# Kernel optimization log

Measured on AMD Instinct MI355X. Metric: run time of the kernel, lower is better.

Reference implementation:

```python
import jax, jax.numpy as jnp
import numpy as np

N = 8192
D_IN = 512
D_HID = 256
D_OUT = 128
NEG_SLOPE = 0.25
MASK_VAL = -1.0e12
EDGE_PROB = 0.004  # avg degree ~33


def _leaky(x):
    return jax.nn.leaky_relu(x, NEG_SLOPE)


def setup_inputs() -> dict:
    key = jax.random.key(0)
    ks = jax.random.split(key, 9)
    x = jax.random.normal(ks[0], (N, D_IN), jnp.float32)
    # sparse-ish normalized adjacency, stored dense (torch uses sparse mm / to_dense)
    vals = jax.random.uniform(ks[1], (N, N), jnp.float32)
    mask = jax.random.uniform(ks[2], (N, N)) < EDGE_PROB
    adj = jnp.where(mask, vals, 0.0).astype(jnp.float32)
    W1 = jax.random.normal(ks[3], (D_IN, D_HID), jnp.float32) * (2.0 / (D_IN + D_HID)) ** 0.5
    b1 = jnp.zeros((D_HID,), jnp.float32)
    W2 = jax.random.normal(ks[4], (D_HID, D_HID), jnp.float32) * (1.0 / D_HID) ** 0.5
    b2 = jnp.zeros((D_HID,), jnp.float32)
    Wg = jax.random.normal(ks[5], (D_HID, D_OUT), jnp.float32) * (2.0 / (D_HID + D_OUT)) ** 0.5
    a = jax.random.normal(ks[6], (2 * D_OUT, 1), jnp.float32) * 0.1
    return dict(x=x, adj=adj, W1=W1, b1=b1, W2=W2, b2=b2, Wg=Wg, a=a)


def reference(x, adj, W1, b1, W2, b2, Wg, a):
    # GCN layer 1: adj @ (x @ W1) + b1, leaky_relu (dropout p=0 / eval -> identity)
    x1 = _leaky(adj @ (x @ W1) + b1)
    # GCN layer 2
    x2 = _leaky(adj @ (x1 @ W2) + b2)
    # GAT layer: h = x2 @ Wg; e[i,j] = leaky_relu([h_i || h_j] @ a)
    # identical to leaky_relu((h@a1)_i + (h@a2)_j) without the O(N^2*2F) concat
    h = x2 @ Wg                              # [N, D_OUT]
    a1 = a[:D_OUT, 0]
    a2 = a[D_OUT:, 0]
    e = _leaky((h @ a1)[:, None] + (h @ a2)[None, :])  # [N, N]
    att = jnp.where(adj > 0, e, MASK_VAL)
    att = jax.nn.softmax(att, axis=1)
    h_prime = att @ h                        # [N, D_OUT] (concat=False -> no elu)
    out = _leaky(h_prime)
    mu = out[:, : D_OUT // 2]
    logvar = out[:, D_OUT // 2 :]
    return mu, logvar
```

## Files before the change

### kernel.cpp

```cpp
#include <hip/hip_runtime.h>

typedef unsigned short u16;
typedef u16 u16x4 __attribute__((ext_vector_type(4)));
typedef __bf16 bf16x8 __attribute__((ext_vector_type(8)));
typedef float f32x4 __attribute__((ext_vector_type(4)));

#define NROW 8192
#define CAP 128
#define D_IN 512
#define D_HID 256
#define D_OUT 128

__device__ __forceinline__ float leaky_f(float x) { return x > 0.f ? x : 0.25f * x; }

__device__ __forceinline__ u16 f2bf_rne(float f) {
  unsigned u = __float_as_uint(f);
  u += 0x7fffu + ((u >> 16) & 1u);
  return (u16)(u >> 16);
}
__device__ __forceinline__ float bf2f(u16 v) { return __uint_as_float(((unsigned)v) << 16); }
__device__ __forceinline__ void split_bf16(float f, u16& hi, u16& lo) {
  hi = f2bf_rne(f);
  float fh = __uint_as_float(((unsigned)hi) << 16);
  lo = f2bf_rne(f - fh);
}

__global__ __launch_bounds__(256) void k_packw(
    const float* __restrict__ W1, u16* __restrict__ B1,
    const float* __restrict__ W2, u16* __restrict__ B2,
    const float* __restrict__ Wg, u16* __restrict__ B3) {
  const float* W; u16* Bt; int K, Nc, idx;
  int pb = blockIdx.x;
  if (pb < 64)      { W = W1; Bt = B1; K = D_IN;  Nc = D_HID; idx = pb * 256 + threadIdx.x; }
  else if (pb < 96) { W = W2; Bt = B2; K = D_HID; Nc = D_HID; idx = (pb - 64) * 256 + threadIdx.x; }
  else              { W = Wg; Bt = B3; K = D_HID; Nc = D_OUT; idx = (pb - 96) * 256 + threadIdx.x; }
  int ko8 = K >> 3;
  int n = idx / ko8, k0 = (idx % ko8) << 3;
  alignas(16) u16 hh[8], ll[8];
#pragma unroll
  for (int j = 0; j < 8; ++j) {
    float f = W[(size_t)(k0 + j) * Nc + n];
    split_bf16(f, hh[j], ll[j]);
  }
  size_t ro = (size_t)n * 2 * K;
  *(uint4*)(Bt + ro + k0)     = *(const uint4*)hh;
  *(uint4*)(Bt + ro + K + k0) = *(const uint4*)ll;
}

__global__ __launch_bounds__(256) void k_csr_gemm1(const float* __restrict__ adj,
    int* __restrict__ cnt, int* __restrict__ cols, float* __restrict__ vals,
    const float* __restrict__ X, const u16* __restrict__ Bt, u16* __restrict__ C) {
  __shared__ alignas(16) u16 Ah[64 * 40], Al[64 * 40];
  __shared__ alignas(16) u16 Bh[64 * 40], Bl[64 * 40];
  __shared__ int csrc;
  int b = blockIdx.x;
  int tid = threadIdx.x;
  if (b < 512) {
    const int N = D_HID, K = D_IN;
    int bm = (b >> 2) * 64, bn = (b & 3) * 64;
    int wave = tid >> 6, lane = tid & 63, l15 = lane & 15, quad = lane >> 4;
    f32x4 acc[4] = {};
    int ar = tid >> 2, aj = (tid & 3) << 3;
    const float* Xrow = X + (size_t)(bm + ar) * K + aj;
    const u16* Brow = Bt + (size_t)(bn + ar) * (2 * K) + aj;
    for (int k0 = 0; k0 < K; k0 += 32) {
      alignas(16) u16 hh[8], ll[8];
      float xv[8];
      *(float4*)(xv)     = *(const float4*)(Xrow + k0);
      *(float4*)(xv + 4) = *(const float4*)(Xrow + k0 + 4);
#pragma unroll
      for (int e = 0; e < 8; ++e) split_bf16(xv[e], hh[e], ll[e]);
      *(uint4*)(&Ah[ar * 40 + aj]) = *(const uint4*)hh;
      *(uint4*)(&Al[ar * 40 + aj]) = *(const uint4*)ll;
      *(uint4*)(&Bh[ar * 40 + aj]) = *(const uint4*)(Brow + k0);
      *(uint4*)(&Bl[ar * 40 + aj]) = *(const uint4*)(Brow + K + k0);
      __syncthreads();
      bf16x8 afh = *(const bf16x8*)(&Ah[(wave * 16 + l15) * 40 + quad * 8]);
      bf16x8 afl = *(const bf16x8*)(&Al[(wave * 16 + l15) * 40 + quad * 8]);
#pragma unroll
      for (int c = 0; c < 4; ++c) {
        bf16x8 bfh = *(const bf16x8*)(&Bh[(c * 16 + l15) * 40 + quad * 8]);
        bf16x8 bfl = *(const bf16x8*)(&Bl[(c * 16 + l15) * 40 + quad * 8]);
        acc[c] = __builtin_amdgcn_mfma_f32_16x16x32_bf16(afh, bfh, acc[c], 0, 0, 0);
        acc[c] = __builtin_amdgcn_mfma_f32_16x16x32_bf16(afh, bfl, acc[c], 0, 0, 0);
        acc[c] = __builtin_amdgcn_mfma_f32_16x16x32_bf16(afl, bfh, acc[c], 0, 0, 0);
      }
      __syncthreads();
    }
#pragma unroll
    for (int c = 0; c < 4; ++c)
#pragma unroll
      for (int rg = 0; rg < 4; ++rg) {
        int rowi = bm + wave * 16 + quad * 4 + rg;
        int coli = bn + c * 16 + l15;
        C[(size_t)rowi * N + coli] = f2bf_rne(acc[c][rg]);
      }
    return;
  }
  int i = b - 512;
  if (tid == 0) csrc = 0;
  __syncthreads();
  int lane = tid & 63;
  const float4* row = (const float4*)(adj + (size_t)i * NROW);
  for (int j4 = tid; j4 < NROW / 4; j4 += 256) {
    float4 v = row[j4];
    int base = j4 * 4;
    bool p0 = v.x > 0.f, p1 = v.y > 0.f, p2 = v.z > 0.f, p3 = v.w > 0.f;
    unsigned long long m0 = __ballot(p0), m1 = __ballot(p1);
    unsigned long long m2 = __ballot(p2), m3 = __ballot(p3);
    int c0 = __popcll(m0), c1 = __popcll(m1), c2 = __popcll(m2), c3 = __popcll(m3);
    int tot = c0 + c1 + c2 + c3;
    if (tot) {
      int wbase = 0;
      if (lane == 0) wbase = atomicAdd(&csrc, tot);
      wbase = __shfl(wbase, 0);
      unsigned long long lm = (1ULL << lane) - 1ULL;
      int o0 = wbase + __popcll(m0 & lm);
      int o1 = wbase + c0 + __popcll(m1 & lm);
      int o2 = wbase + c0 + c1 + __popcll(m2 & lm);
      int o3 = wbase + c0 + c1 + c2 + __popcll(m3 & lm);
      if (p0 && o0 < CAP) { cols[i*CAP+o0] = base;   vals[i*CAP+o0] = v.x; }
      if (p1 && o1 < CAP) { cols[i*CAP+o1] = base+1; vals[i*CAP+o1] = v.y; }
      if (p2 && o2 < CAP) { cols[i*CAP+o2] = base+2; vals[i*CAP+o2] = v.z; }
      if (p3 && o3 < CAP) { cols[i*CAP+o3] = base+3; vals[i*CAP+o3] = v.w; }
    }
  }
  __syncthreads();
  if (tid == 0) cnt[i] = (csrc < CAP) ? csrc : CAP;
}


__device__ __forceinline__ float4 gather_row256(const u16* __restrict__ Hin,
    const int* scw, const float* svw, int n, int lane) {
  float4 acc = {0.f, 0.f, 0.f, 0.f};
  int k = 0;
  for (; k + 7 < n; k += 8) {
    int   c0 = scw[k],     c1 = scw[k + 1], c2 = scw[k + 2], c3 = scw[k + 3];
    int   c4 = scw[k + 4], c5 = scw[k + 5], c6 = scw[k + 6], c7 = scw[k + 7];
    float w0 = svw[k],     w1 = svw[k + 1], w2 = svw[k + 2], w3 = svw[k + 3];
    float w4 = svw[k + 4], w5 = svw[k + 5], w6 = svw[k + 6], w7 = svw[k + 7];
    u16x4 v0 = *(const u16x4*)(Hin + (size_t)c0 * 256 + 4 * lane);
    u16x4 v1 = *(const u16x4*)(Hin + (size_t)c1 * 256 + 4 * lane);
    u16x4 v2 = *(const u16x4*)(Hin + (size_t)c2 * 256 + 4 * lane);
    u16x4 v3 = *(const u16x4*)(Hin + (size_t)c3 * 256 + 4 * lane);
    u16x4 v4 = *(const u16x4*)(Hin + (size_t)c4 * 256 + 4 * lane);
    u16x4 v5 = *(const u16x4*)(Hin + (size_t)c5 * 256 + 4 * lane);
    u16x4 v6 = *(const u16x4*)(Hin + (size_t)c6 * 256 + 4 * lane);
    u16x4 v7 = *(const u16x4*)(Hin + (size_t)c7 * 256 + 4 * lane);
    acc.x = fmaf(w0, bf2f(v0[0]), acc.x); acc.y = fmaf(w0, bf2f(v0[1]), acc.y);
    acc.z = fmaf(w0, bf2f(v0[2]), acc.z); acc.w = fmaf(w0, bf2f(v0[3]), acc.w);
    acc.x = fmaf(w1, bf2f(v1[0]), acc.x); acc.y = fmaf(w1, bf2f(v1[1]), acc.y);
    acc.z = fmaf(w1, bf2f(v1[2]), acc.z); acc.w = fmaf(w1, bf2f(v1[3]), acc.w);
    acc.x = fmaf(w2, bf2f(v2[0]), acc.x); acc.y = fmaf(w2, bf2f(v2[1]), acc.y);
    acc.z = fmaf(w2, bf2f(v2[2]), acc.z); acc.w = fmaf(w2, bf2f(v2[3]), acc.w);
    acc.x = fmaf(w3, bf2f(v3[0]), acc.x); acc.y = fmaf(w3, bf2f(v3[1]), acc.y);
    acc.z = fmaf(w3, bf2f(v3[2]), acc.z); acc.w = fmaf(w3, bf2f(v3[3]), acc.w);
    acc.x = fmaf(w4, bf2f(v4[0]), acc.x); acc.y = fmaf(w4, bf2f(v4[1]), acc.y);
    acc.z = fmaf(w4, bf2f(v4[2]), acc.z); acc.w = fmaf(w4, bf2f(v4[3]), acc.w);
    acc.x = fmaf(w5, bf2f(v5[0]), acc.x); acc.y = fmaf(w5, bf2f(v5[1]), acc.y);
    acc.z = fmaf(w5, bf2f(v5[2]), acc.z); acc.w = fmaf(w5, bf2f(v5[3]), acc.w);
    acc.x = fmaf(w6, bf2f(v6[0]), acc.x); acc.y = fmaf(w6, bf2f(v6[1]), acc.y);
    acc.z = fmaf(w6, bf2f(v6[2]), acc.z); acc.w = fmaf(w6, bf2f(v6[3]), acc.w);
    acc.x = fmaf(w7, bf2f(v7[0]), acc.x); acc.y = fmaf(w7, bf2f(v7[1]), acc.y);
    acc.z = fmaf(w7, bf2f(v7[2]), acc.z); acc.w = fmaf(w7, bf2f(v7[3]), acc.w);
  }
  for (; k < n; ++k) {
    float wv = svw[k];
    u16x4 v = *(const u16x4*)(Hin + (size_t)scw[k] * 256 + 4 * lane);
    acc.x = fmaf(wv, bf2f(v[0]), acc.x); acc.y = fmaf(wv, bf2f(v[1]), acc.y);
    acc.z = fmaf(wv, bf2f(v[2]), acc.z); acc.w = fmaf(wv, bf2f(v[3]), acc.w);
  }
  return acc;
}

__global__ __launch_bounds__(256) void k_fuse1(const u16* __restrict__ Hin,
    const float* __restrict__ bias, const int* __restrict__ cnt,
    const int* __restrict__ cols, const float* __restrict__ vals,
    const u16* __restrict__ Bt, u16* __restrict__ Cout) {
  __shared__ alignas(16) u16 AhF[8 * 16 * 40], AlF[8 * 16 * 40];
  __shared__ int   sc[4 * CAP];
  __shared__ float sv[4 * CAP];
  int tid = threadIdx.x;
  int wave = tid >> 6, lane = tid & 63, l15 = lane & 15, quad = lane >> 4;
  int bm = blockIdx.x * 16;
  int* scw = sc + wave * CAP;
  float* svw = sv + wave * CAP;
  float4 bv = ((const float4*)bias)[lane];
#pragma unroll
  for (int rr = 0; rr < 4; ++rr) {
    int r = wave * 4 + rr;
    int i = bm + r;
    int n = cnt[i];
    if (lane < n)      { scw[lane]      = cols[i*CAP+lane];      svw[lane]      = vals[i*CAP+lane]; }
    if (lane + 64 < n) { scw[lane + 64] = cols[i*CAP+lane+64];   svw[lane + 64] = vals[i*CAP+lane+64]; }
    float4 acc = gather_row256(Hin, scw, svw, n, lane);
    float r4[4] = { leaky_f(acc.x + bv.x), leaky_f(acc.y + bv.y),
                    leaky_f(acc.z + bv.z), leaky_f(acc.w + bv.w) };
    u16x4 hi4, lo4;
#pragma unroll
    for (int e = 0; e < 4; ++e) { u16 hh, ll; split_bf16(r4[e], hh, ll); hi4[e] = hh; lo4[e] = ll; }
    int dst = (lane >> 3) * 640 + r * 40 + (lane & 7) * 4;
    *(u16x4*)(&AhF[dst]) = hi4;
    *(u16x4*)(&AlF[dst]) = lo4;
  }
  __syncthreads();
#pragma unroll
  for (int hN = 0; hN < 2; ++hN) {
    f32x4 acc[2] = {};
#pragma unroll
    for (int k0 = 0; k0 < D_HID; k0 += 32) {
      bf16x8 afh = *(const bf16x8*)(&AhF[(k0 >> 5) * 640 + l15 * 40 + quad * 8]);
      bf16x8 afl = *(const bf16x8*)(&AlF[(k0 >> 5) * 640 + l15 * 40 + quad * 8]);
#pragma unroll
      for (int c = 0; c < 2; ++c) {
        int col = hN * 128 + wave * 32 + c * 16 + l15;
        const u16* bp = Bt + (size_t)col * (2 * D_HID) + k0 + quad * 8;
        bf16x8 bfh = *(const bf16x8*)(bp);
        bf16x8 bfl = *(const bf16x8*)(bp + D_HID);
        acc[c] = __builtin_amdgcn_mfma_f32_16x16x32_bf16(afh, bfh, acc[c], 0, 0, 0);
        acc[c] = __builtin_amdgcn_mfma_f32_16x16x32_bf16(afh, bfl, acc[c], 0, 0, 0);
        acc[c] = __builtin_amdgcn_mfma_f32_16x16x32_bf16(afl, bfh, acc[c], 0, 0, 0);
      }
    }
#pragma unroll
    for (int c = 0; c < 2; ++c)
#pragma unroll
      for (int rg = 0; rg < 4; ++rg) {
        int rowi = bm + quad * 4 + rg;
        int coli = hN * 128 + wave * 32 + c * 16 + l15;
        Cout[(size_t)rowi * 256 + coli] = f2bf_rne(acc[c][rg]);
      }
  }
}

__global__ __launch_bounds__(256) void k_fuse2(const u16* __restrict__ Hin,
    const float* __restrict__ bias, const int* __restrict__ cnt,
    const int* __restrict__ cols, const float* __restrict__ vals,
    const u16* __restrict__ Bt, u16* __restrict__ Hb,
    const float* __restrict__ aptr, float* __restrict__ s1, float* __restrict__ s2) {
  __shared__ alignas(16) u16 AhF[8 * 16 * 40], AlF[8 * 16 * 40];
  __shared__ int   sc[4 * CAP];
  __shared__ float sv[4 * CAP];
  __shared__ float sp1[4][16], sp2[4][16];
  int tid = threadIdx.x;
  int wave = tid >> 6, lane = tid & 63, l15 = lane & 15, quad = lane >> 4;
  int bm = blockIdx.x * 16;
  int* scw = sc + wave * CAP;
  float* svw = sv + wave * CAP;
  float4 bv = ((const float4*)bias)[lane];
#pragma unroll
  for (int rr = 0; rr < 4; ++rr) {
    int r = wave * 4 + rr;
    int i = bm + r;
    int n = cnt[i];
    if (lane < n)      { scw[lane]      = cols[i*CAP+lane];      svw[lane]      = vals[i*CAP+lane]; }
    if (lane + 64 < n) { scw[lane + 64] = cols[i*CAP+lane+64];   svw[lane + 64] = vals[i*CAP+lane+64]; }
    float4 acc = gather_row256(Hin, scw, svw, n, lane);
    float r4[4] = { leaky_f(acc.x + bv.x), leaky_f(acc.y + bv.y),
                    leaky_f(acc.z + bv.z), leaky_f(acc.w + bv.w) };
    u16x4 hi4, lo4;
#pragma unroll
    for (int e = 0; e < 4; ++e) { u16 hh, ll; split_bf16(r4[e], hh, ll); hi4[e] = hh; lo4[e] = ll; }
    int dst = (lane >> 3) * 640 + r * 40 + (lane & 7) * 4;
    *(u16x4*)(&AhF[dst]) = hi4;
    *(u16x4*)(&AlF[dst]) = lo4;
  }
  __syncthreads();
  f32x4 acc[2] = {};
#pragma unroll
  for (int k0 = 0; k0 < D_HID; k0 += 32) {
    bf16x8 afh = *(const bf16x8*)(&AhF[(k0 >> 5) * 640 + l15 * 40 + quad * 8]);
    bf16x8 afl = *(const bf16x8*)(&AlF[(k0 >> 5) * 640 + l15 * 40 + quad * 8]);
#pragma unroll
    for (int c = 0; c < 2; ++c) {
      int col = wave * 32 + c * 16 + l15;
      const u16* bp = Bt + (size_t)col * (2 * D_HID) + k0 + quad * 8;
      bf16x8 bfh = *(const bf16x8*)(bp);
      bf16x8 bfl = *(const bf16x8*)(bp + D_HID);
      acc[c] = __builtin_amdgcn_mfma_f32_16x16x32_bf16(afh, bfh, acc[c], 0, 0, 0);
      acc[c] = __builtin_amdgcn_mfma_f32_16x16x32_bf16(afh, bfl, acc[c], 0, 0, 0);
      acc[c] = __builtin_amdgcn_mfma_f32_16x16x32_bf16(afl, bfh, acc[c], 0, 0, 0);
    }
  }
#pragma unroll
  for (int c = 0; c < 2; ++c)
#pragma unroll
    for (int rg = 0; rg < 4; ++rg) {
      int rowi = bm + quad * 4 + rg;
      int coli = wave * 32 + c * 16 + l15;
      Hb[(size_t)rowi * 128 + coli] = f2bf_rne(acc[c][rg]);
    }
  float a1v[2], a2v[2];
#pragma unroll
  for (int c = 0; c < 2; ++c) {
    a1v[c] = aptr[wave * 32 + c * 16 + l15];
    a2v[c] = aptr[128 + wave * 32 + c * 16 + l15];
  }
#pragma unroll
  for (int rg = 0; rg < 4; ++rg) {
    float p1 = 0.f, p2 = 0.f;
#pragma unroll
    for (int c = 0; c < 2; ++c) { p1 = fmaf(acc[c][rg], a1v[c], p1); p2 = fmaf(acc[c][rg], a2v[c], p2); }
#pragma unroll
    for (int m = 1; m < 16; m <<= 1) { p1 += __shfl_xor(p1, m); p2 += __shfl_xor(p2, m); }
    if (l15 == 0) {
      int rloc = quad * 4 + rg;
      sp1[wave][rloc] = p1; sp2[wave][rloc] = p2;
    }
  }
  __syncthreads();
  if (tid < 16) {
    s1[bm + tid] = sp1[0][tid] + sp1[1][tid] + sp1[2][tid] + sp1[3][tid];
    s2[bm + tid] = sp2[0][tid] + sp2[1][tid] + sp2[2][tid] + sp2[3][tid];
  }
}

__global__ __launch_bounds__(256) void k_attn(const u16* __restrict__ Hb,
    const float* __restrict__ s1, const float* __restrict__ s2,
    const int* __restrict__ cnt, const int* __restrict__ cols, float* __restrict__ out) {
  __shared__ int sc[4][CAP];
  __shared__ float sp[4][CAP];
  int w = threadIdx.x >> 6, lane = threadIdx.x & 63;
  int i = blockIdx.x * 4 + w;
  int n = cnt[i];
  float s1i = s1[i];
  float e0 = -1e30f, e1 = -1e30f;
  if (lane < n)      { int c = cols[i * CAP + lane];      sc[w][lane]      = c; e0 = leaky_f(s1i + s2[c]); }
  if (lane + 64 < n) { int c = cols[i * CAP + lane + 64]; sc[w][lane + 64] = c; e1 = leaky_f(s1i + s2[c]); }
  float m = fmaxf(e0, e1);
#pragma unroll
  for (int o = 32; o > 0; o >>= 1) m = fmaxf(m, __shfl_xor(m, o));
  float p0 = (lane < n)      ? expf(e0 - m) : 0.f;
  float p1 = (lane + 64 < n) ? expf(e1 - m) : 0.f;
  if (lane < n)      sp[w][lane]      = p0;
  if (lane + 64 < n) sp[w][lane + 64] = p1;
  float s = p0 + p1;
#pragma unroll
  for (int o = 32; o > 0; o >>= 1) s += __shfl_xor(s, o);
  float inv = (n > 0) ? 1.0f / s : 0.f;
  __syncthreads();
  int half = lane >> 5, t32 = lane & 31;
  float4 acc = {0.f, 0.f, 0.f, 0.f};
  int k = half;
  for (; k + 6 < n; k += 8) {
    int   c0 = sc[w][k],     c1 = sc[w][k + 2], c2 = sc[w][k + 4], c3 = sc[w][k + 6];
    float w0 = sp[w][k],     w1 = sp[w][k + 2], w2 = sp[w][k + 4], w3 = sp[w][k + 6];
    u16x4 a0 = *(const u16x4*)(Hb + (size_t)c0 * 128 + 4 * t32);
    u16x4 a1 = *(const u16x4*)(Hb + (size_t)c1 * 128 + 4 * t32);
    u16x4 a2 = *(const u16x4*)(Hb + (size_t)c2 * 128 + 4 * t32);
    u16x4 a3 = *(const u16x4*)(Hb + (size_t)c3 * 128 + 4 * t32);
    acc.x = fmaf(w0, bf2f(a0[0]), acc.x); acc.y = fmaf(w0, bf2f(a0[1]), acc.y);
    acc.z = fmaf(w0, bf2f(a0[2]), acc.z); acc.w = fmaf(w0, bf2f(a0[3]), acc.w);
    acc.x = fmaf(w1, bf2f(a1[0]), acc.x); acc.y = fmaf(w1, bf2f(a1[1]), acc.y);
    acc.z = fmaf(w1, bf2f(a1[2]), acc.z); acc.w = fmaf(w1, bf2f(a1[3]), acc.w);
    acc.x = fmaf(w2, bf2f(a2[0]), acc.x); acc.y = fmaf(w2, bf2f(a2[1]), acc.y);
    acc.z = fmaf(w2, bf2f(a2[2]), acc.z); acc.w = fmaf(w2, bf2f(a2[3]), acc.w);
    acc.x = fmaf(w3, bf2f(a3[0]), acc.x); acc.y = fmaf(w3, bf2f(a3[1]), acc.y);
    acc.z = fmaf(w3, bf2f(a3[2]), acc.z); acc.w = fmaf(w3, bf2f(a3[3]), acc.w);
  }
  for (; k < n; k += 2) {
    float wv = sp[w][k];
    u16x4 a = *(const u16x4*)(Hb + (size_t)sc[w][k] * 128 + 4 * t32);
    acc.x = fmaf(wv, bf2f(a[0]), acc.x); acc.y = fmaf(wv, bf2f(a[1]), acc.y);
    acc.z = fmaf(wv, bf2f(a[2]), acc.z); acc.w = fmaf(wv, bf2f(a[3]), acc.w);
  }
  acc.x += __shfl_xor(acc.x, 32);
  acc.y += __shfl_xor(acc.y, 32);
  acc.z += __shfl_xor(acc.z, 32);
  acc.w += __shfl_xor(acc.w, 32);
  if (lane < 32) {
    float4 r;
    r.x = leaky_f(acc.x * inv);
    r.y = leaky_f(acc.y * inv);
    r.z = leaky_f(acc.z * inv);
    r.w = leaky_f(acc.w * inv);
    float4* o4 = (float4*)out;
    if (lane < 16) o4[(size_t)i * 16 + lane] = r;
    else           o4[(size_t)NROW * 16 + (size_t)i * 16 + (lane - 16)] = r;
  }
}

extern "C" void kernel_launch(void* const* d_in, const int* in_sizes, int n_in,
                              void* d_out, int out_size, void* d_ws, size_t ws_size,
                              hipStream_t stream) {
  const float* x   = (const float*)d_in[0];
  const float* adj = (const float*)d_in[1];
  const float* W1  = (const float*)d_in[2];
  const float* b1  = (const float*)d_in[3];
  const float* W2  = (const float*)d_in[4];
  const float* b2  = (const float*)d_in[5];
  const float* Wg  = (const float*)d_in[6];
  const float* a   = (const float*)d_in[7];
  float* out = (float*)d_out;

  char* ws = (char*)d_ws;
  int*   row_cnt  = (int*)  (ws + 0);
  int*   row_cols = (int*)  (ws + 32768);
  float* row_vals = (float*)(ws + 4227072);
  u16*   B1t      = (u16*)  (ws + 8421376);
  u16*   B2t      = (u16*)  (ws + 8945664);
  u16*   B3t      = (u16*)  (ws + 9207808);
  float* s1       = (float*)(ws + 9338880);
  float* s2       = (float*)(ws + 9371648);
  u16*   hbf      = (u16*)  (ws + 9404416);
  u16*   H0T2     = (u16*)  (ws + 13598720);
  u16*   T2       = (u16*)  (ws + 21987328);

  k_packw<<<112, 256, 0, stream>>>(W1, B1t, W2, B2t, Wg, B3t);
  k_csr_gemm1<<<512 + NROW, 256, 0, stream>>>(adj, row_cnt, row_cols, row_vals, x, B1t, H0T2);
  k_fuse1<<<NROW / 16, 256, 0, stream>>>(H0T2, b1, row_cnt, row_cols, row_vals, B2t, T2);
  k_fuse2<<<NROW / 16, 256, 0, stream>>>(T2, b2, row_cnt, row_cols, row_vals, B3t, hbf, a, s1, s2);
  k_attn<<<NROW / 4, 256, 0, stream>>>(hbf, s1, s2, row_cnt, row_cols, out);
}
```

Measured before the change: 447.3 us.

## Use 512-thread blocks in fused SpMM+GEMM kernels, two rows per wave

Both fused layer kernels now launch 8 waves per block instead of 4. Each wave gathers two sparse rows instead of four, and the dense MFMA stage is split across 8 waves by column. Layer 1 no longer loops over two column halves, and layer 2 computes one 16-column tile per wave with an 8-way reduction for the attention scores. The aim is more memory-level parallelism and shorter serial gather chains per wave, at the cost of more shared memory per block and possibly lower block occupancy.

```diff
diff --git a/kernel.cpp b/kernel.cpp
--- a/kernel.cpp
+++ b/kernel.cpp
@@ -173,98 +173,42 @@
   return acc;
 }
 
-__global__ __launch_bounds__(256) void k_fuse1(const u16* __restrict__ Hin,
+__device__ __forceinline__ void spmm_row_to_lds(const u16* __restrict__ Hin,
+    const int* scw, const float* svw, int n, int lane, float4 bv,
+    u16* AhF, u16* AlF, int r) {
+  float4 acc = gather_row256(Hin, scw, svw, n, lane);
+  float r4[4] = { leaky_f(acc.x + bv.x), leaky_f(acc.y + bv.y),
+                  leaky_f(acc.z + bv.z), leaky_f(acc.w + bv.w) };
+  u16x4 hi4, lo4;
+#pragma unroll
+  for (int e = 0; e < 4; ++e) { u16 hh, ll; split_bf16(r4[e], hh, ll); hi4[e] = hh; lo4[e] = ll; }
+  int dst = (lane >> 3) * 640 + r * 40 + (lane & 7) * 4;
+  *(u16x4*)(&AhF[dst]) = hi4;
+  *(u16x4*)(&AlF[dst]) = lo4;
+}
+
+__global__ __launch_bounds__(512) void k_fuse1(const u16* __restrict__ Hin,
     const float* __restrict__ bias, const int* __restrict__ cnt,
     const int* __restrict__ cols, const float* __restrict__ vals,
     const u16* __restrict__ Bt, u16* __restrict__ Cout) {
   __shared__ alignas(16) u16 AhF[8 * 16 * 40], AlF[8 * 16 * 40];
-  __shared__ int   sc[4 * CAP];
-  __shared__ float sv[4 * CAP];
+  __shared__ int   sc[16 * CAP];
+  __shared__ float sv[16 * CAP];
   int tid = threadIdx.x;
   int wave = tid >> 6, lane = tid & 63, l15 = lane & 15, quad = lane >> 4;
   int bm = blockIdx.x * 16;
-  int* scw = sc + wave * CAP;
-  float* svw = sv + wave * CAP;
+  int r0 = wave * 2, r1 = r0 + 1;
+  int i0 = bm + r0, i1 = bm + r1;
+  int n0 = cnt[i0], n1 = cnt[i1];
+  int* sc0 = sc + r0 * CAP;  float* sv0 = sv + r0 * CAP;
+  int* sc1 = sc + r1 * CAP;  float* sv1 = sv + r1 * CAP;
+  if (lane < n0)      { sc0[lane]      = cols[i0*CAP+lane];    sv0[lane]      = vals[i0*CAP+lane]; }
+  if (lane + 64 < n0) { sc0[lane + 64] = cols[i0*CAP+lane+64]; sv0[lane + 64] = vals[i0*CAP+lane+64]; }
+  if (lane < n1)      { sc1[lane]      = cols[i1*CAP+lane];    sv1[lane]      = vals[i1*CAP+lane]; }
+  if (lane + 64 < n1) { sc1[lane + 64] = cols[i1*CAP+lane+64]; sv1[lane + 64] = vals[i1*CAP+lane+64]; }
   float4 bv = ((const float4*)bias)[lane];
-#pragma unroll
-  for (int rr = 0; rr < 4; ++rr) {
-    int r = wave * 4 + rr;
-    int i = bm + r;
-    int n = cnt[i];
-    if (lane < n)      { scw[lane]      = cols[i*CAP+lane];      svw[lane]      = vals[i*CAP+lane]; }
-    if (lane + 64 < n) { scw[lane + 64] = cols[i*CAP+lane+64];   svw[lane + 64] = vals[i*CAP+lane+64]; }
-    float4 acc = gather_row256(Hin, scw, svw, n, lane);
-    float r4[4] = { leaky_f(acc.x + bv.x), leaky_f(acc.y + bv.y),
-                    leaky_f(acc.z + bv.z), leaky_f(acc.w + bv.w) };
-    u16x4 hi4, lo4;
-#pragma unroll
-    for (int e = 0; e < 4; ++e) { u16 hh, ll; split_bf16(r4[e], hh, ll); hi4[e] = hh; lo4[e] = ll; }
-    int dst = (lane >> 3) * 640 + r * 40 + (lane & 7) * 4;
-    *(u16x4*)(&AhF[dst]) = hi4;
-    *(u16x4*)(&AlF[dst]) = lo4;
-  }
-  __syncthreads();
-#pragma unroll
-  for (int hN = 0; hN < 2; ++hN) {
-    f32x4 acc[2] = {};
-#pragma unroll
-    for (int k0 = 0; k0 < D_HID; k0 += 32) {
-      bf16x8 afh = *(const bf16x8*)(&AhF[(k0 >> 5) * 640 + l15 * 40 + quad * 8]);
-      bf16x8 afl = *(const bf16x8*)(&AlF[(k0 >> 5) * 640 + l15 * 40 + quad * 8]);
-#pragma unroll
-      for (int c = 0; c < 2; ++c) {
-        int col = hN * 128 + wave * 32 + c * 16 + l15;
-        const u16* bp = Bt + (size_t)col * (2 * D_HID) + k0 + quad * 8;
-        bf16x8 bfh = *(const bf16x8*)(bp);
-        bf16x8 bfl = *(const bf16x8*)(bp + D_HID);
-        acc[c] = __builtin_amdgcn_mfma_f32_16x16x32_bf16(afh, bfh, acc[c], 0, 0, 0);
-        acc[c] = __builtin_amdgcn_mfma_f32_16x16x32_bf16(afh, bfl, acc[c], 0, 0, 0);
-        acc[c] = __builtin_amdgcn_mfma_f32_16x16x32_bf16(afl, bfh, acc[c], 0, 0, 0);
-      }
-    }
-#pragma unroll
-    for (int c = 0; c < 2; ++c)
-#pragma unroll
-      for (int rg = 0; rg < 4; ++rg) {
-        int rowi = bm + quad * 4 + rg;
-        int coli = hN * 128 + wave * 32 + c * 16 + l15;
-        Cout[(size_t)rowi * 256 + coli] = f2bf_rne(acc[c][rg]);
-      }
-  }
-}
-
-__global__ __launch_bounds__(256) void k_fuse2(const u16* __restrict__ Hin,
-    const float* __restrict__ bias, const int* __restrict__ cnt,
-    const int* __restrict__ cols, const float* __restrict__ vals,
-    const u16* __restrict__ Bt, u16* __restrict__ Hb,
-    const float* __restrict__ aptr, float* __restrict__ s1, float* __restrict__ s2) {
-  __shared__ alignas(16) u16 AhF[8 * 16 * 40], AlF[8 * 16 * 40];
-  __shared__ int   sc[4 * CAP];
-  __shared__ float sv[4 * CAP];
-  __shared__ float sp1[4][16], sp2[4][16];
-  int tid = threadIdx.x;
-  int wave = tid >> 6, lane = tid & 63, l15 = lane & 15, quad = lane >> 4;
-  int bm = blockIdx.x * 16;
-  int* scw = sc + wave * CAP;
-  float* svw = sv + wave * CAP;
-  float4 bv = ((const float4*)bias)[lane];
-#pragma unroll
-  for (int rr = 0; rr < 4; ++rr) {
-    int r = wave * 4 + rr;
-    int i = bm + r;
-    int n = cnt[i];
-    if (lane < n)      { scw[lane]      = cols[i*CAP+lane];      svw[lane]      = vals[i*CAP+lane]; }
-    if (lane + 64 < n) { scw[lane + 64] = cols[i*CAP+lane+64];   svw[lane + 64] = vals[i*CAP+lane+64]; }
-    float4 acc = gather_row256(Hin, scw, svw, n, lane);
-    float r4[4] = { leaky_f(acc.x + bv.x), leaky_f(acc.y + bv.y),
-                    leaky_f(acc.z + bv.z), leaky_f(acc.w + bv.w) };
-    u16x4 hi4, lo4;
-#pragma unroll
-    for (int e = 0; e < 4; ++e) { u16 hh, ll; split_bf16(r4[e], hh, ll); hi4[e] = hh; lo4[e] = ll; }
-    int dst = (lane >> 3) * 640 + r * 40 + (lane & 7) * 4;
-    *(u16x4*)(&AhF[dst]) = hi4;
-    *(u16x4*)(&AlF[dst]) = lo4;
-  }
+  spmm_row_to_lds(Hin, sc0, sv0, n0, lane, bv, AhF, AlF, r0);
+  spmm_row_to_lds(Hin, sc1, sv1, n1, lane, bv, AhF, AlF, r1);
   __syncthreads();
   f32x4 acc[2] = {};
 #pragma unroll
@@ -288,19 +232,60 @@
     for (int rg = 0; rg < 4; ++rg) {
       int rowi = bm + quad * 4 + rg;
       int coli = wave * 32 + c * 16 + l15;
-      Hb[(size_t)rowi * 128 + coli] = f2bf_rne(acc[c][rg]);
+      Cout[(size_t)rowi * 256 + coli] = f2bf_rne(acc[c][rg]);
     }
-  float a1v[2], a2v[2];
-#pragma unroll
-  for (int c = 0; c < 2; ++c) {
-    a1v[c] = aptr[wave * 32 + c * 16 + l15];
-    a2v[c] = aptr[128 + wave * 32 + c * 16 + l15];
+}
+
+__global__ __launch_bounds__(512) void k_fuse2(const u16* __restrict__ Hin,
+    const float* __restrict__ bias, const int* __restrict__ cnt,
+    const int* __restrict__ cols, const float* __restrict__ vals,
+    const u16* __restrict__ Bt, u16* __restrict__ Hb,
+    const float* __restrict__ aptr, float* __restrict__ s1, float* __restrict__ s2) {
+  __shared__ alignas(16) u16 AhF[8 * 16 * 40], AlF[8 * 16 * 40];
+  __shared__ int   sc[16 * CAP];
+  __shared__ float sv[16 * CAP];
+  __shared__ float sp1[8][16], sp2[8][16];
+  int tid = threadIdx.x;
+  int wave = tid >> 6, lane = tid & 63, l15 = lane & 15, quad = lane >> 4;
+  int bm = blockIdx.x * 16;
+  int r0 = wave * 2, r1 = r0 + 1;
+  int i0 = bm + r0, i1 = bm + r1;
+  int n0 = cnt[i0], n1 = cnt[i1];
+  int* sc0 = sc + r0 * CAP;  float* sv0 = sv + r0 * CAP;
+  int* sc1 = sc + r1 * CAP;  float* sv1 = sv + r1 * CAP;
+  if (lane < n0)      { sc0[lane]      = cols[i0*CAP+lane];    sv0[lane]      = vals[i0*CAP+lane]; }
+  if (lane + 64 < n0) { sc0[lane + 64] = cols[i0*CAP+lane+64]; sv0[lane + 64] = vals[i0*CAP+lane+64]; }
+  if (lane < n1)      { sc1[lane]      = cols[i1*CAP+lane];    sv1[lane]      = vals[i1*CAP+lane]; }
+  if (lane + 64 < n1) { sc1[lane + 64] = cols[i1*CAP+lane+64]; sv1[lane + 64] = vals[i1*CAP+lane+64]; }
+  float4 bv = ((const float4*)bias)[lane];
+  spmm_row_to_lds(Hin, sc0, sv0, n0, lane, bv, AhF, AlF, r0);
+  spmm_row_to_lds(Hin, sc1, sv1, n1, lane, bv, AhF, AlF, r1);
+  __syncthreads();
+  f32x4 acc = {};
+#pragma unroll
+  for (int k0 = 0; k0 < D_HID; k0 += 32) {
+    bf16x8 afh = *(const bf16x8*)(&AhF[(k0 >> 5) * 640 + l15 * 40 + quad * 8]);
+    bf16x8 afl = *(const bf16x8*)(&AlF[(k0 >> 5) * 640 + l15 * 40 + quad * 8]);
+    int col = wave * 16 + l15;
+    const u16* bp = Bt + (size_t)col * (2 * D_HID) + k0 + quad * 8;
+    bf16x8 bfh = *(const bf16x8*)(bp);
+    bf16x8 bfl = *(const bf16x8*)(bp + D_HID);
+    acc = __builtin_amdgcn_mfma_f32_16x16x32_bf16(afh, bfh, acc, 0, 0, 0);
+    acc = __builtin_amdgcn_mfma_f32_16x16x32_bf16(afh, bfl, acc, 0, 0, 0);
+    acc = __builtin_amdgcn_mfma_f32_16x16x32_bf16(afl, bfh, acc, 0, 0, 0);
   }
 #pragma unroll
   for (int rg = 0; rg < 4; ++rg) {
-    float p1 = 0.f, p2 = 0.f;
-#pragma unroll
-    for (int c = 0; c < 2; ++c) { p1 = fmaf(acc[c][rg], a1v[c], p1); p2 = fmaf(acc[c][rg], a2v[c], p2); }
+    int rowi = bm + quad * 4 + rg;
+    int coli = wave * 16 + l15;
+    Hb[(size_t)rowi * 128 + coli] = f2bf_rne(acc[rg]);
+  }
+  float a1v = aptr[wave * 16 + l15];
+  float a2v = aptr[128 + wave * 16 + l15];
+#pragma unroll
+  for (int rg = 0; rg < 4; ++rg) {
+    float p1 = acc[rg] * a1v;
+    float p2 = acc[rg] * a2v;
 #pragma unroll
     for (int m = 1; m < 16; m <<= 1) { p1 += __shfl_xor(p1, m); p2 += __shfl_xor(p2, m); }
     if (l15 == 0) {
@@ -310,8 +295,11 @@
   }
   __syncthreads();
   if (tid < 16) {
-    s1[bm + tid] = sp1[0][tid] + sp1[1][tid] + sp1[2][tid] + sp1[3][tid];
-    s2[bm + tid] = sp2[0][tid] + sp2[1][tid] + sp2[2][tid] + sp2[3][tid];
+    float t1 = 0.f, t2 = 0.f;
+#pragma unroll
+    for (int wv = 0; wv < 8; ++wv) { t1 += sp1[wv][tid]; t2 += sp2[wv][tid]; }
+    s1[bm + tid] = t1;
+    s2[bm + tid] = t2;
   }
 }
 
@@ -408,7 +396,7 @@
 
   k_packw<<<112, 256, 0, stream>>>(W1, B1t, W2, B2t, Wg, B3t);
   k_csr_gemm1<<<512 + NROW, 256, 0, stream>>>(adj, row_cnt, row_cols, row_vals, x, B1t, H0T2);
-  k_fuse1<<<NROW / 16, 256, 0, stream>>>(H0T2, b1, row_cnt, row_cols, row_vals, B2t, T2);
-  k_fuse2<<<NROW / 16, 256, 0, stream>>>(T2, b2, row_cnt, row_cols, row_vals, B3t, hbf, a, s1, s2);
+  k_fuse1<<<NROW / 16, 512, 0, stream>>>(H0T2, b1, row_cnt, row_cols, row_vals, B2t, T2);
+  k_fuse2<<<NROW / 16, 512, 0, stream>>>(T2, b2, row_cnt, row_cols, row_vals, B3t, hbf, a, s1, s2);
   k_attn<<<NROW / 4, 256, 0, stream>>>(hbf, s1, s2, row_cnt, row_cols, out);
 }
```

Measured after the change: 438.3 us (median of 2 runs). 2.0% less time.
